# Kernel optimization log

Hardware: AMD Instinct MI355X
Metric: run time of the kernel (lower is better)

## Reference

```python
import jax, jax.numpy as jnp
import numpy as np

# Hierarchy: 3 levels with 50 / 500 / 5000 classes, branching factor 10.
PIQUETS = (0, 50, 550, 5550)  # cumulative offsets per level
NB_LEVELS = 3
BATCH = 4096


def _make_parent():
    """parent[j] = global index of the parent of global node j (0 for roots).
    Encodes the same structure as the dense H matrix (H[p, j] = 1 iff parent[j] == p)."""
    parent = np.zeros(PIQUETS[-1], dtype=np.int32)
    parent[PIQUETS[1]:PIQUETS[2]] = np.arange(500) // 10            # level-1 -> level-0
    parent[PIQUETS[2]:PIQUETS[3]] = PIQUETS[1] + np.arange(5000) // 10  # level-2 -> level-1
    return jnp.asarray(parent)


def setup_inputs() -> dict:
    key = jax.random.key(0)
    k1, k2 = jax.random.split(key)
    y_pred = jax.random.normal(k1, (BATCH, PIQUETS[-1]), dtype=jnp.float32)
    target = jax.random.randint(k2, (BATCH,), 0, 5000)  # local leaf-level indices
    return {"y_pred": y_pred, "target": target, "parent": _make_parent()}


def reference(y_pred, target, parent):
    # children_preds[b, p] = sum of child logits of node p
    # == (H[:piquets[-2], :] @ y_pred.T).T, exploiting H's one-parent sparsity.
    children = jax.ops.segment_sum(
        y_pred.T[PIQUETS[1]:], parent[PIQUETS[1]:], num_segments=PIQUETS[-2]
    ).T  # (B, piquets[-2])

    levels_pred = [y_pred[:, PIQUETS[k]:PIQUETS[k + 1]] for k in range(NB_LEVELS)]
    levels_children = [children[:, PIQUETS[k]:PIQUETS[k + 1]] for k in range(NB_LEVELS - 1)]
    log_p = [jax.nn.log_softmax(l, axis=1) for l in levels_pred]
    log_c = [jax.nn.log_softmax(l, axis=1) for l in levels_children]

    # Ancestor targets per level (vectorized replacement for get_grandparents loops)
    g = target.astype(jnp.int32) + PIQUETS[-2]  # global leaf index
    globs = [g]
    for _ in range(NB_LEVELS - 1):
        globs.append(parent[globs[-1]])
    globs = globs[::-1]  # level 0 .. level L-1, global indices
    loc = [globs[k] - PIQUETS[k] for k in range(NB_LEVELS)]  # local per-level targets

    def ce(logp, tgt):
        return -jnp.take_along_axis(logp, tgt[:, None], axis=1).mean()

    def kl_mean(logp, logq):
        # torch KLDivLoss(reduction='mean'): mean over ALL elements of q*(log q - log p)
        return jnp.mean(jnp.exp(logq) * (logq - logp))

    loss = jnp.float32(0.0)
    kl_penalty = jnp.float32(0.0)
    for k in range(NB_LEVELS - 1):
        kl_penalty += 0.5 * (kl_mean(log_p[k], log_c[k]) + kl_mean(log_c[k], log_p[k]))
        loss += 0.5 * ce(log_p[k], loc[k])
    loss += 0.5 * ce(log_p[-1], loc[-1])
    loss += 0.5 * kl_penalty
    return loss
```

## Files before the change

kernel.cpp:

```cpp
#include <hip/hip_runtime.h>

#define BATCH 4096
#define ROW   5550

typedef const __attribute__((address_space(1))) void glb_void;
typedef __attribute__((address_space(3))) void lds_void;

__device__ __forceinline__ float wave_sum(float v) {
    #pragma unroll
    for (int off = 32; off; off >>= 1) v += __shfl_xor(v, off, 64);
    return v;
}

__global__ __launch_bounds__(256)
void hjsd_kernel(const float* __restrict__ y, const int* __restrict__ tgt,
                 float* __restrict__ rowout) {
    __shared__ __align__(16) float s_buf[5552];
    __shared__ float scr[36];

    const int b    = blockIdx.x;
    const int tid  = threadIdx.x;
    const int w    = tid >> 6;
    const int lane = tid & 63;

    const float* yrow  = y + (size_t)b * ROW;
    const int    ofs   = (b & 1) ? 2 : 0;
    const float* gbase = yrow - ofs;

    for (int c = w; c < 22; c += 4) {
        int d = 256 * c + 4 * lane;
        if (d < 5552) {
            __builtin_amdgcn_global_load_lds((glb_void*)(gbase + d),
                                             (lds_void*)(s_buf + 256 * c),
                                             16, 0, 0);
        }
    }
    asm volatile("s_waitcnt vmcnt(0)" ::: "memory");
    __syncthreads();

    const float* s_row = s_buf + ofs;
    const float* s1    = s_row + 50;
    const float* s2    = s_row + 550;

    float E2 = 0.f, EC1 = 0.f, E1 = 0.f, EC0 = 0.f, E0 = 0.f;
    float S11 = 0.f, S21 = 0.f, S10 = 0.f, S20 = 0.f;

    if (tid < 250) {
        const float2* p2 = reinterpret_cast<const float2*>(s2 + 20 * tid);
        float v[20];
        #pragma unroll
        for (int j = 0; j < 10; ++j) { float2 t2 = p2[j]; v[2*j] = t2.x; v[2*j+1] = t2.y; }
        float c0 = 0.f, c1 = 0.f;
        #pragma unroll
        for (int j = 0; j < 10; ++j) c0 += v[j];
        #pragma unroll
        for (int j = 0; j < 10; ++j) c1 += v[10 + j];
        #pragma unroll
        for (int j = 0; j < 20; ++j) E2 += __expf(v[j]);
        float ec0 = __expf(c0), ec1 = __expf(c1);
        EC1 = ec0 + ec1;
        float2 xab = *reinterpret_cast<const float2*>(s1 + 2 * tid);
        float ea = __expf(xab.x), eb = __expf(xab.y);
        E1  = ea + eb;
        S11 = ec0 * (c0 - xab.x) + ec1 * (c1 - xab.y);
        S21 = ea * (xab.x - c0) + eb * (xab.y - c1);
    }

    if (tid < 50) {
        const float2* p1 = reinterpret_cast<const float2*>(s1 + 10 * tid);
        float c = 0.f;
        #pragma unroll
        for (int j = 0; j < 5; ++j) { float2 t2 = p1[j]; c += t2.x + t2.y; }
        float ec = __expf(c);
        float x0 = s_row[tid];
        float e0 = __expf(x0);
        EC0 = ec; E0 = e0;
        S10 = ec * (c - x0);
        S20 = e0 * (x0 - c);
    }

    float sums[9] = {E2, EC1, E1, EC0, E0, S11, S21, S10, S20};
    #pragma unroll
    for (int k = 0; k < 9; ++k) sums[k] = wave_sum(sums[k]);
    if (lane == 0) {
        #pragma unroll
        for (int k = 0; k < 9; ++k) scr[w * 9 + k] = sums[k];
    }
    __syncthreads();

    if (tid == 0) {
        float t9[9];
        #pragma unroll
        for (int k = 0; k < 9; ++k)
            t9[k] = scr[k] + scr[9 + k] + scr[18 + k] + scr[27 + k];
        float L2 = __logf(t9[0]), L1 = __logf(t9[2]), L0 = __logf(t9[4]);
        int t = tgt[b];
        float ce = (L2 - s2[t]) + (L1 - s1[t / 10]) + (L0 - s_row[t / 100]);
        float kl = (0.25f / 500.0f) * (t9[5] / t9[1] + t9[6] / t9[2])
                 + (0.25f / 50.0f)  * (t9[7] / t9[3] + t9[8] / t9[4]);
        rowout[b] = 0.5f * ce + kl;
    }
}

__global__ __launch_bounds__(256)
void reduce_kernel(const float* __restrict__ rows, float* __restrict__ out) {
    __shared__ float scr[4];
    const int tid = threadIdx.x;
    const float4* p = reinterpret_cast<const float4*>(rows);
    float s = 0.0f;
    #pragma unroll
    for (int i = 0; i < 4; ++i) {
        float4 v = p[tid + 256 * i];
        s += v.x + v.y + v.z + v.w;
    }
    s = wave_sum(s);
    if ((tid & 63) == 0) scr[tid >> 6] = s;
    __syncthreads();
    if (tid == 0) out[0] = (scr[0] + scr[1] + scr[2] + scr[3]) * (1.0f / BATCH);
}

extern "C" void kernel_launch(void* const* d_in, const int* in_sizes, int n_in,
                              void* d_out, int out_size, void* d_ws, size_t ws_size,
                              hipStream_t stream) {
    const float* y   = (const float*)d_in[0];
    const int*   tgt = (const int*)d_in[1];
    float* out    = (float*)d_out;
    float* rowbuf = (float*)d_ws;

    hjsd_kernel<<<BATCH, 256, 0, stream>>>(y, tgt, rowbuf);
    reduce_kernel<<<1, 256, 0, stream>>>(rowbuf, out);
}
```

Before: 137.2 us.

## Process eight rows per block with double-buffered async LDS staging

Each block now handles eight batch rows instead of one. It double-buffers the row loads into LDS with global_load_lds so the next row's transfer overlaps the current row's exp and reduction work. Per-row results are accumulated in-block, so the final reduce kernel sums only 512 partials. The trade-off is fewer blocks (512 over 256 CUs) and twice the LDS per block, which may lower occupancy and latency hiding compared with the many-block launch.

New measurement: 140.9 us. 1.03x slower.

```diff
diff --git a/kernel.cpp b/kernel.cpp
--- a/kernel.cpp
+++ b/kernel.cpp
@@ -2,6 +2,9 @@
 
 #define BATCH 4096
 #define ROW   5550
+#define RPB   8
+#define GRID  (BATCH / RPB)
+#define WSPAN 1388
 
 typedef const __attribute__((address_space(1))) void glb_void;
 typedef __attribute__((address_space(3))) void lds_void;
@@ -14,105 +17,121 @@
 
 __global__ __launch_bounds__(256)
 void hjsd_kernel(const float* __restrict__ y, const int* __restrict__ tgt,
-                 float* __restrict__ rowout) {
-    __shared__ __align__(16) float s_buf[5552];
+                 float* __restrict__ blockout) {
+    __shared__ __align__(16) float s_buf[2][5552];
     __shared__ float scr[36];
+    __shared__ int   s_tgt[RPB];
 
     const int b    = blockIdx.x;
     const int tid  = threadIdx.x;
     const int w    = tid >> 6;
     const int lane = tid & 63;
 
-    const float* yrow  = y + (size_t)b * ROW;
-    const int    ofs   = (b & 1) ? 2 : 0;
-    const float* gbase = yrow - ofs;
+    if (tid < RPB) s_tgt[tid] = tgt[RPB * b + tid];
 
-    for (int c = w; c < 22; c += 4) {
-        int d = 256 * c + 4 * lane;
-        if (d < 5552) {
-            __builtin_amdgcn_global_load_lds((glb_void*)(gbase + d),
-                                             (lds_void*)(s_buf + 256 * c),
-                                             16, 0, 0);
+    auto stage = [&](int r, int buf) {
+        const int g = RPB * b + r;
+        const float* gb = y + (size_t)g * ROW - ((g & 1) ? 2 : 0);
+        const float* gw = gb + WSPAN * w;
+        float*       lw = s_buf[buf] + WSPAN * w;
+        #pragma unroll
+        for (int c = 0; c < 5; ++c)
+            __builtin_amdgcn_global_load_lds((glb_void*)(gw + 256 * c + 4 * lane),
+                                             (lds_void*)(lw + 256 * c), 16, 0, 0);
+        if (lane < 27)
+            __builtin_amdgcn_global_load_lds((glb_void*)(gw + 1280 + 4 * lane),
+                                             (lds_void*)(lw + 1280), 16, 0, 0);
+    };
+
+    stage(0, 0);
+    float rowacc = 0.0f;
+
+    for (int r = 0; r < RPB; ++r) {
+        const int cur = r & 1;
+        if (r < RPB - 1) {
+            stage(r + 1, cur ^ 1);
+            asm volatile("s_waitcnt vmcnt(6)" ::: "memory");
+        } else {
+            asm volatile("s_waitcnt vmcnt(0)" ::: "memory");
+        }
+        __builtin_amdgcn_sched_barrier(0);
+        __builtin_amdgcn_s_barrier();
+
+        const float* s_row = s_buf[cur] + ((r & 1) ? 2 : 0);
+        const float* s1    = s_row + 50;
+        const float* s2    = s_row + 550;
+
+        float E2 = 0.f, EC1 = 0.f, E1 = 0.f, EC0 = 0.f, E0 = 0.f;
+        float S11 = 0.f, S21 = 0.f, S10 = 0.f, S20 = 0.f;
+
+        if (tid < 250) {
+            const float2* p2 = reinterpret_cast<const float2*>(s2 + 20 * tid);
+            float v[20];
+            #pragma unroll
+            for (int j = 0; j < 10; ++j) { float2 t2 = p2[j]; v[2*j] = t2.x; v[2*j+1] = t2.y; }
+            float c0 = 0.f, c1 = 0.f;
+            #pragma unroll
+            for (int j = 0; j < 10; ++j) c0 += v[j];
+            #pragma unroll
+            for (int j = 0; j < 10; ++j) c1 += v[10 + j];
+            #pragma unroll
+            for (int j = 0; j < 20; ++j) E2 += __expf(v[j]);
+            float ec0 = __expf(c0), ec1 = __expf(c1);
+            EC1 = ec0 + ec1;
+            float2 xab = *reinterpret_cast<const float2*>(s1 + 2 * tid);
+            float ea = __expf(xab.x), eb = __expf(xab.y);
+            E1  = ea + eb;
+            S11 = ec0 * (c0 - xab.x) + ec1 * (c1 - xab.y);
+            S21 = ea * (xab.x - c0) + eb * (xab.y - c1);
+        }
+        if (tid < 50) {
+            const float2* p1 = reinterpret_cast<const float2*>(s1 + 10 * tid);
+            float c = 0.f;
+            #pragma unroll
+            for (int j = 0; j < 5; ++j) { float2 t2 = p1[j]; c += t2.x + t2.y; }
+            float ec = __expf(c);
+            float x0 = s_row[tid];
+            float e0 = __expf(x0);
+            EC0 = ec; E0 = e0;
+            S10 = ec * (c - x0);
+            S20 = e0 * (x0 - c);
+        }
+        float ysum = 0.f;
+        if (tid == 0) {
+            int t = s_tgt[r];
+            ysum = s2[t] + s1[t / 10] + s_row[t / 100];
+        }
+
+        float sums[9] = {E2, EC1, E1, EC0, E0, S11, S21, S10, S20};
+        #pragma unroll
+        for (int k = 0; k < 9; ++k) sums[k] = wave_sum(sums[k]);
+        if (lane == 0) {
+            #pragma unroll
+            for (int k = 0; k < 9; ++k) scr[w * 9 + k] = sums[k];
+        }
+        asm volatile("s_waitcnt lgkmcnt(0)" ::: "memory");
+        __builtin_amdgcn_sched_barrier(0);
+        __builtin_amdgcn_s_barrier();
+
+        if (tid == 0) {
+            float t9[9];
+            #pragma unroll
+            for (int k = 0; k < 9; ++k)
+                t9[k] = scr[k] + scr[9 + k] + scr[18 + k] + scr[27 + k];
+            float ce = __logf(t9[0]) + __logf(t9[2]) + __logf(t9[4]) - ysum;
+            float kl = (0.25f / 500.0f) * (t9[5] / t9[1] + t9[6] / t9[2])
+                     + (0.25f / 50.0f)  * (t9[7] / t9[3] + t9[8] / t9[4]);
+            rowacc += 0.5f * ce + kl;
         }
     }
-    asm volatile("s_waitcnt vmcnt(0)" ::: "memory");
-    __syncthreads();
-
-    const float* s_row = s_buf + ofs;
-    const float* s1    = s_row + 50;
-    const float* s2    = s_row + 550;
-
-    float E2 = 0.f, EC1 = 0.f, E1 = 0.f, EC0 = 0.f, E0 = 0.f;
-    float S11 = 0.f, S21 = 0.f, S10 = 0.f, S20 = 0.f;
-
-    if (tid < 250) {
-        const float2* p2 = reinterpret_cast<const float2*>(s2 + 20 * tid);
-        float v[20];
-        #pragma unroll
-        for (int j = 0; j < 10; ++j) { float2 t2 = p2[j]; v[2*j] = t2.x; v[2*j+1] = t2.y; }
-        float c0 = 0.f, c1 = 0.f;
-        #pragma unroll
-        for (int j = 0; j < 10; ++j) c0 += v[j];
-        #pragma unroll
-        for (int j = 0; j < 10; ++j) c1 += v[10 + j];
-        #pragma unroll
-        for (int j = 0; j < 20; ++j) E2 += __expf(v[j]);
-        float ec0 = __expf(c0), ec1 = __expf(c1);
-        EC1 = ec0 + ec1;
-        float2 xab = *reinterpret_cast<const float2*>(s1 + 2 * tid);
-        float ea = __expf(xab.x), eb = __expf(xab.y);
-        E1  = ea + eb;
-        S11 = ec0 * (c0 - xab.x) + ec1 * (c1 - xab.y);
-        S21 = ea * (xab.x - c0) + eb * (xab.y - c1);
-    }
-
-    if (tid < 50) {
-        const float2* p1 = reinterpret_cast<const float2*>(s1 + 10 * tid);
-        float c = 0.f;
-        #pragma unroll
-        for (int j = 0; j < 5; ++j) { float2 t2 = p1[j]; c += t2.x + t2.y; }
-        float ec = __expf(c);
-        float x0 = s_row[tid];
-        float e0 = __expf(x0);
-        EC0 = ec; E0 = e0;
-        S10 = ec * (c - x0);
-        S20 = e0 * (x0 - c);
-    }
-
-    float sums[9] = {E2, EC1, E1, EC0, E0, S11, S21, S10, S20};
-    #pragma unroll
-    for (int k = 0; k < 9; ++k) sums[k] = wave_sum(sums[k]);
-    if (lane == 0) {
-        #pragma unroll
-        for (int k = 0; k < 9; ++k) scr[w * 9 + k] = sums[k];
-    }
-    __syncthreads();
-
-    if (tid == 0) {
-        float t9[9];
-        #pragma unroll
-        for (int k = 0; k < 9; ++k)
-            t9[k] = scr[k] + scr[9 + k] + scr[18 + k] + scr[27 + k];
-        float L2 = __logf(t9[0]), L1 = __logf(t9[2]), L0 = __logf(t9[4]);
-        int t = tgt[b];
-        float ce = (L2 - s2[t]) + (L1 - s1[t / 10]) + (L0 - s_row[t / 100]);
-        float kl = (0.25f / 500.0f) * (t9[5] / t9[1] + t9[6] / t9[2])
-                 + (0.25f / 50.0f)  * (t9[7] / t9[3] + t9[8] / t9[4]);
-        rowout[b] = 0.5f * ce + kl;
-    }
+    if (tid == 0) blockout[b] = rowacc;
 }
 
 __global__ __launch_bounds__(256)
 void reduce_kernel(const float* __restrict__ rows, float* __restrict__ out) {
     __shared__ float scr[4];
     const int tid = threadIdx.x;
-    const float4* p = reinterpret_cast<const float4*>(rows);
-    float s = 0.0f;
-    #pragma unroll
-    for (int i = 0; i < 4; ++i) {
-        float4 v = p[tid + 256 * i];
-        s += v.x + v.y + v.z + v.w;
-    }
+    float s = rows[tid] + rows[tid + 256];
     s = wave_sum(s);
     if ((tid & 63) == 0) scr[tid >> 6] = s;
     __syncthreads();
@@ -124,9 +143,9 @@
                               hipStream_t stream) {
     const float* y   = (const float*)d_in[0];
     const int*   tgt = (const int*)d_in[1];
-    float* out    = (float*)d_out;
-    float* rowbuf = (float*)d_ws;
+    float* out      = (float*)d_out;
+    float* blockbuf = (float*)d_ws;
 
-    hjsd_kernel<<<BATCH, 256, 0, stream>>>(y, tgt, rowbuf);
-    reduce_kernel<<<1, 256, 0, stream>>>(rowbuf, out);
+    hjsd_kernel<<<GRID, 256, 0, stream>>>(y, tgt, blockbuf);
+    reduce_kernel<<<1, 256, 0, stream>>>(blockbuf, out);
 }
```

## Drop in-block cross-wave reduction, write per-wave partials, reduce in extra kernels

Applied to the files above, without the earlier changes.

The main kernel no longer runs a second __syncthreads and single-thread finalisation. Each wave instead writes its nine partial sums plus the target logit sum to a per-row workspace slot, and two new reduction kernels finish the log/divide math and the batch mean. The LDS fill is restructured so each wave loads a contiguous 1388-float span, the target index is prefetched before the wait, and the LDS read order is rotated per thread to reduce bank conflicts. The cost is an extra kernel launch and about 786 KB of additional workspace traffic.

New measurement: 139.2 us. Within noise of the previous version (+1.5%).

```diff
diff --git a/kernel.cpp b/kernel.cpp
--- a/kernel.cpp
+++ b/kernel.cpp
@@ -2,6 +2,7 @@
 
 #define BATCH 4096
 #define ROW   5550
+#define WSPAN 1388
 
 typedef const __attribute__((address_space(1))) void glb_void;
 typedef __attribute__((address_space(3))) void lds_void;
@@ -14,26 +15,29 @@
 
 __global__ __launch_bounds__(256)
 void hjsd_kernel(const float* __restrict__ y, const int* __restrict__ tgt,
-                 float* __restrict__ rowout) {
+                 float* __restrict__ P) {
     __shared__ __align__(16) float s_buf[5552];
-    __shared__ float scr[36];
 
     const int b    = blockIdx.x;
     const int tid  = threadIdx.x;
     const int w    = tid >> 6;
     const int lane = tid & 63;
 
-    const float* yrow  = y + (size_t)b * ROW;
-    const int    ofs   = (b & 1) ? 2 : 0;
-    const float* gbase = yrow - ofs;
+    int t = 0;
+    if (tid == 0) t = tgt[b];
 
-    for (int c = w; c < 22; c += 4) {
-        int d = 256 * c + 4 * lane;
-        if (d < 5552) {
-            __builtin_amdgcn_global_load_lds((glb_void*)(gbase + d),
-                                             (lds_void*)(s_buf + 256 * c),
-                                             16, 0, 0);
-        }
+    const int    ofs = (b & 1) ? 2 : 0;
+    const float* gb  = y + (size_t)b * ROW - ofs;
+    {
+        const float* gw = gb + WSPAN * w;
+        float*       lw = s_buf + WSPAN * w;
+        #pragma unroll
+        for (int c = 0; c < 5; ++c)
+            __builtin_amdgcn_global_load_lds((glb_void*)(gw + 256 * c + 4 * lane),
+                                             (lds_void*)(lw + 256 * c), 16, 0, 0);
+        if (lane < 27)
+            __builtin_amdgcn_global_load_lds((glb_void*)(gw + 1280 + 4 * lane),
+                                             (lds_void*)(lw + 1280), 16, 0, 0);
     }
     asm volatile("s_waitcnt vmcnt(0)" ::: "memory");
     __syncthreads();
@@ -42,21 +46,22 @@
     const float* s1    = s_row + 50;
     const float* s2    = s_row + 550;
 
-    float E2 = 0.f, EC1 = 0.f, E1 = 0.f, EC0 = 0.f, E0 = 0.f;
-    float S11 = 0.f, S21 = 0.f, S10 = 0.f, S20 = 0.f;
+    float E2=0.f, EC1=0.f, E1=0.f, EC0=0.f, E0=0.f;
+    float S11=0.f, S21=0.f, S10=0.f, S20=0.f, Y=0.f;
 
     if (tid < 250) {
-        const float2* p2 = reinterpret_cast<const float2*>(s2 + 20 * tid);
-        float v[20];
-        #pragma unroll
-        for (int j = 0; j < 10; ++j) { float2 t2 = p2[j]; v[2*j] = t2.x; v[2*j+1] = t2.y; }
+        const float2* g0 = reinterpret_cast<const float2*>(s2 + 20 * tid);
+        const float2* g1 = g0 + 5;
+        const int r = tid % 5;
         float c0 = 0.f, c1 = 0.f;
         #pragma unroll
-        for (int j = 0; j < 10; ++j) c0 += v[j];
-        #pragma unroll
-        for (int j = 0; j < 10; ++j) c1 += v[10 + j];
-        #pragma unroll
-        for (int j = 0; j < 20; ++j) E2 += __expf(v[j]);
+        for (int j = 0; j < 5; ++j) {
+            int s = r + j; if (s >= 5) s -= 5;
+            float2 a = g0[s], d = g1[s];
+            c0 += a.x + a.y;
+            c1 += d.x + d.y;
+            E2 += __expf(a.x) + __expf(a.y) + __expf(d.x) + __expf(d.y);
+        }
         float ec0 = __expf(c0), ec1 = __expf(c1);
         EC1 = ec0 + ec1;
         float2 xab = *reinterpret_cast<const float2*>(s1 + 2 * tid);
@@ -68,9 +73,14 @@
 
     if (tid < 50) {
         const float2* p1 = reinterpret_cast<const float2*>(s1 + 10 * tid);
+        const int r = tid % 5;
         float c = 0.f;
         #pragma unroll
-        for (int j = 0; j < 5; ++j) { float2 t2 = p1[j]; c += t2.x + t2.y; }
+        for (int j = 0; j < 5; ++j) {
+            int s = r + j; if (s >= 5) s -= 5;
+            float2 a = p1[s];
+            c += a.x + a.y;
+        }
         float ec = __expf(c);
         float x0 = s_row[tid];
         float e0 = __expf(x0);
@@ -79,44 +89,50 @@
         S20 = e0 * (x0 - c);
     }
 
+    if (tid == 0) Y = s2[t] + s1[t / 10] + s_row[t / 100];
+
     float sums[9] = {E2, EC1, E1, EC0, E0, S11, S21, S10, S20};
     #pragma unroll
     for (int k = 0; k < 9; ++k) sums[k] = wave_sum(sums[k]);
+
     if (lane == 0) {
-        #pragma unroll
-        for (int k = 0; k < 9; ++k) scr[w * 9 + k] = sums[k];
-    }
-    __syncthreads();
-
-    if (tid == 0) {
-        float t9[9];
-        #pragma unroll
-        for (int k = 0; k < 9; ++k)
-            t9[k] = scr[k] + scr[9 + k] + scr[18 + k] + scr[27 + k];
-        float L2 = __logf(t9[0]), L1 = __logf(t9[2]), L0 = __logf(t9[4]);
-        int t = tgt[b];
-        float ce = (L2 - s2[t]) + (L1 - s1[t / 10]) + (L0 - s_row[t / 100]);
-        float kl = (0.25f / 500.0f) * (t9[5] / t9[1] + t9[6] / t9[2])
-                 + (0.25f / 50.0f)  * (t9[7] / t9[3] + t9[8] / t9[4]);
-        rowout[b] = 0.5f * ce + kl;
+        float* dst = P + (size_t)b * 48 + 12 * w;
+        *reinterpret_cast<float4*>(dst)     = make_float4(sums[0], sums[1], sums[2], sums[3]);
+        *reinterpret_cast<float4*>(dst + 4) = make_float4(sums[4], sums[5], sums[6], sums[7]);
+        *reinterpret_cast<float2*>(dst + 8) = make_float2(sums[8], Y);
     }
 }
 
 __global__ __launch_bounds__(256)
-void reduce_kernel(const float* __restrict__ rows, float* __restrict__ out) {
+void reduce1(const float* __restrict__ P, float* __restrict__ part) {
     __shared__ float scr[4];
     const int tid = threadIdx.x;
-    const float4* p = reinterpret_cast<const float4*>(rows);
-    float s = 0.0f;
+    const int b   = blockIdx.x * 256 + tid;
+    const float4* q4 = reinterpret_cast<const float4*>(P + (size_t)b * 48);
+    float t9[10];
     #pragma unroll
-    for (int i = 0; i < 4; ++i) {
-        float4 v = p[tid + 256 * i];
-        s += v.x + v.y + v.z + v.w;
+    for (int k = 0; k < 10; ++k) t9[k] = 0.f;
+    #pragma unroll
+    for (int w = 0; w < 4; ++w) {
+        float4 A = q4[3 * w], B = q4[3 * w + 1], C = q4[3 * w + 2];
+        t9[0] += A.x; t9[1] += A.y; t9[2] += A.z; t9[3] += A.w;
+        t9[4] += B.x; t9[5] += B.y; t9[6] += B.z; t9[7] += B.w;
+        t9[8] += C.x; t9[9] += C.y;
     }
+    float loss = 0.5f * (__logf(t9[0]) + __logf(t9[2]) + __logf(t9[4]) - t9[9])
+               + (0.25f / 500.0f) * (t9[5] / t9[1] + t9[6] / t9[2])
+               + (0.25f / 50.0f)  * (t9[7] / t9[3] + t9[8] / t9[4]);
+    loss = wave_sum(loss);
+    if ((tid & 63) == 0) scr[tid >> 6] = loss;
+    __syncthreads();
+    if (tid == 0) part[blockIdx.x] = scr[0] + scr[1] + scr[2] + scr[3];
+}
+
+__global__ __launch_bounds__(64)
+void reduce2(const float* __restrict__ part, float* __restrict__ out) {
+    float s = (threadIdx.x < 16) ? part[threadIdx.x] : 0.f;
     s = wave_sum(s);
-    if ((tid & 63) == 0) scr[tid >> 6] = s;
-    __syncthreads();
-    if (tid == 0) out[0] = (scr[0] + scr[1] + scr[2] + scr[3]) * (1.0f / BATCH);
+    if (threadIdx.x == 0) out[0] = s * (1.0f / BATCH);
 }
 
 extern "C" void kernel_launch(void* const* d_in, const int* in_sizes, int n_in,
@@ -124,9 +140,11 @@
                               hipStream_t stream) {
     const float* y   = (const float*)d_in[0];
     const int*   tgt = (const int*)d_in[1];
-    float* out    = (float*)d_out;
-    float* rowbuf = (float*)d_ws;
+    float* out  = (float*)d_out;
+    float* P    = (float*)d_ws;
+    float* part = (float*)d_ws + (size_t)BATCH * 48;
 
-    hjsd_kernel<<<BATCH, 256, 0, stream>>>(y, tgt, rowbuf);
-    reduce_kernel<<<1, 256, 0, stream>>>(rowbuf, out);
+    hjsd_kernel<<<BATCH, 256, 0, stream>>>(y, tgt, P);
+    reduce1<<<16, 256, 0, stream>>>(P, part);
+    reduce2<<<1, 64, 0, stream>>>(part, out);
 }
```
